# Kernel tuning notes

Hardware: AMD Instinct MI355X
Metric: run time of the kernel (lower is better)

## Reference

```python
import jax, jax.numpy as jnp
import numpy as np

EPS = 1e-7  # K.epsilon()
NUM_ROUTING = 3


def squash(v, axis=-1):
    sq = jnp.sum(jnp.square(v), axis=axis, keepdims=True)
    return sq / (1.0 + sq) * (v / jnp.sqrt(sq + EPS))


def setup_inputs() -> dict:
    key = jax.random.key(0)
    k1, k2 = jax.random.split(key)
    B, NI, DI = 256, 1152, 8   # batch, input_num_capsule, input_dim_vector
    NJ, DJ = 10, 16            # num_capsule, dim_vector
    u = jax.random.normal(k1, (B, NI, DI), dtype=jnp.float32)
    W = jax.random.normal(k2, (NJ, NI, DJ, DI), dtype=jnp.float32) * 0.1
    return {"u": u, "W": W}


def reference(u, W):
    # u_hat[b,j,i,d] = sum_k u[b,i,k] * W[j,i,d,k]  (replaces tile + batch_dot)
    u_hat = jnp.einsum('bik,jidk->bjid', u, W)
    B, NJ, NI, _ = u_hat.shape
    b_ij = jnp.zeros((B, NJ, NI), dtype=u_hat.dtype)
    v_j = None
    for _ in range(NUM_ROUTING):
        c_ij = jax.nn.softmax(b_ij, axis=1)            # softmax over output capsules (dim=1)
        s_j = jnp.einsum('bji,bjid->bjd', c_ij, u_hat)  # weighted sum over input capsules
        v_j = squash(s_j)                               # (B, NJ, DJ)
        b_ij = b_ij + jnp.einsum('bjd,bjid->bji', v_j, u_hat)  # agreement update
    return v_j
```

## Files before the change

### kernel.cpp

```cpp
#include <hip/hip_runtime.h>
#include <math.h>

#define BB   256
#define NI   1152
#define DI   8
#define NJ   10
#define DJ   16
#define NCHUNK 18
#define CHUNK  64
#define BG     32
#define NBG    8
#define GRID_MAIN (NJ * NCHUNK * NBG)
#define CTP  66

typedef _Float16 half2_t __attribute__((ext_vector_type(2)));
typedef _Float16 half4_t __attribute__((ext_vector_type(4)));
typedef _Float16 half8_t __attribute__((ext_vector_type(8)));
typedef float    f32x4   __attribute__((ext_vector_type(4)));

template <int CTRL>
__device__ __forceinline__ float dpp_add(float x) {
    int xi = __float_as_int(x);
    int yi = __builtin_amdgcn_update_dpp(0, xi, CTRL, 0xF, 0xF, true);
    return x + __int_as_float(yi);
}

__device__ __forceinline__ float dot16(half8_t w, half8_t uu) {
    half2_t w0 = {w[0], w[1]}, w1 = {w[2], w[3]}, w2 = {w[4], w[5]}, w3 = {w[6], w[7]};
    half2_t a0 = {uu[0], uu[1]}, a1 = {uu[2], uu[3]}, a2 = {uu[4], uu[5]}, a3 = {uu[6], uu[7]};
    float acc = __builtin_amdgcn_fdot2(w0, a0, 0.f, false);
    acc = __builtin_amdgcn_fdot2(w1, a1, acc, false);
    acc = __builtin_amdgcn_fdot2(w2, a2, acc, false);
    acc = __builtin_amdgcn_fdot2(w3, a3, acc, false);
    return acc;
}

struct Ctx {
    int j, chunk, bg, i0, b0, tid, il, dq, lane, w, g, xcd, local;
};

__device__ __forceinline__ Ctx make_ctx(int bid, int tid) {
    Ctx c;
    c.xcd = bid & 7; c.local = bid >> 3;
    int gx = c.xcd * (GRID_MAIN / 8) + c.local;
    c.j = gx % NJ; int r = gx / NJ;
    c.chunk = r % NCHUNK; c.bg = r / NCHUNK;
    c.i0 = c.chunk * CHUNK; c.b0 = c.bg * BG;
    c.tid = tid; c.il = tid >> 2; c.dq = tid & 3;
    c.lane = tid & 63; c.w = tid >> 6; c.g = (c.lane >> 4) & 3;
    return c;
}

__device__ __forceinline__ void loadW16(const _Float16* __restrict__ W16, const Ctx& cx,
                                        half8_t* Wh) {
    const half8_t* wp = (const half8_t*)(W16 +
        (((size_t)cx.j * NI + cx.i0 + cx.il) * DJ + cx.dq * 4) * DI);
#pragma unroll
    for (int q = 0; q < 4; ++q) Wh[q] = wp[q];
}

__global__ __launch_bounds__(256) void k_cvt(const float* __restrict__ uf,
                                             const float* __restrict__ Wf,
                                             _Float16* __restrict__ u16,
                                             _Float16* __restrict__ W16) {
    int idx = blockIdx.x * 256 + threadIdx.x;
    const int nu4 = (BB * NI * DI) / 4;
    const int nw4 = (NJ * NI * DJ * DI) / 4;
    if (idx < nu4) {
        float4 v = ((const float4*)uf)[idx];
        half4_t h = {(_Float16)v.x, (_Float16)v.y, (_Float16)v.z, (_Float16)v.w};
        ((half4_t*)u16)[idx] = h;
    } else if (idx < nu4 + nw4) {
        int k = idx - nu4;
        float4 v = ((const float4*)Wf)[k];
        half4_t h = {(_Float16)v.x, (_Float16)v.y, (_Float16)v.z, (_Float16)v.w};
        ((half4_t*)W16)[k] = h;
    }
}

template <int CSRC>
__device__ __forceinline__ void phaseAm(const Ctx& cx, const _Float16* __restrict__ u16,
                                        const _Float16* __restrict__ W16,
                                        float* __restrict__ spart,
                                        const float* ctile, float* sres2) {
    int l = cx.lane, w = cx.w;
    int drow = l & 15;
    int ksub = l >> 4;

    half8_t Wf[4];
#pragma unroll
    for (int qq = 0; qq < 4; ++qq) {
        int i = cx.i0 + w * 16 + qq * 4 + ksub;
        Wf[qq] = *(const half8_t*)(W16 + (((size_t)cx.j * NI + i) * DJ + drow) * DI);
    }

    half8_t au[2][4];
#pragma unroll
    for (int h = 0; h < 2; ++h) {
        int b = cx.b0 + h * 16 + drow;
#pragma unroll
        for (int qq = 0; qq < 4; ++qq) {
            int il = w * 16 + qq * 4 + ksub;
            au[h][qq] = *(const half8_t*)(u16 + ((size_t)b * NI + cx.i0 + il) * DI);
        }
    }
    if (CSRC == 1) {
#pragma unroll
        for (int h = 0; h < 2; ++h) {
#pragma unroll
            for (int qq = 0; qq < 4; ++qq) {
                int il = w * 16 + qq * 4 + ksub;
                _Float16 ch = (_Float16)ctile[(h * 16 + drow) * CTP + il];
                half8_t cc = {ch, ch, ch, ch, ch, ch, ch, ch};
                au[h][qq] = au[h][qq] * cc;
            }
        }
    }

#pragma unroll
    for (int h = 0; h < 2; ++h) {
        f32x4 acc = {0.f, 0.f, 0.f, 0.f};
#pragma unroll
        for (int qq = 0; qq < 4; ++qq)
            acc = __builtin_amdgcn_mfma_f32_16x16x32_f16(au[h][qq], Wf[qq], acc, 0, 0, 0);
#pragma unroll
        for (int r = 0; r < 4; ++r)
            sres2[((h * 4 + w) * 16 + ksub * 4 + r) * 17 + drow] = acc[r];
    }
    __syncthreads();

#pragma unroll
    for (int p = 0; p < 2; ++p) {
        int idx = p * 256 + cx.tid;
        int d = idx & 15, brow = (idx >> 4) & 15, h = idx >> 8;
        float s = 0.f;
#pragma unroll
        for (int w2 = 0; w2 < 4; ++w2)
            s += sres2[((h * 4 + w2) * 16 + brow) * 17 + d];
        if (CSRC == 0) s *= 0.1f;
        spart[(((size_t)cx.chunk * BB + cx.b0 + h * 16 + brow) * NJ + cx.j) * DJ + d] = s;
    }
}

__global__ __launch_bounds__(256) void k_A0m(const _Float16* __restrict__ u16,
                                             const _Float16* __restrict__ W16,
                                             float* __restrict__ spart) {
    __shared__ __align__(16) float sres2[2 * 4 * 16 * 17];
    Ctx cx = make_ctx(blockIdx.x, threadIdx.x);
    phaseAm<0>(cx, u16, W16, spart, nullptr, sres2);
}

__global__ __launch_bounds__(256) void k_Afm(const _Float16* __restrict__ u16,
                                             const _Float16* __restrict__ W16,
                                             const _Float16* __restrict__ delta,
                                             float* __restrict__ spart) {
    __shared__ __align__(16) float sres2[2 * 4 * 16 * 17];
    __shared__ __align__(16) float ctile[BG * CTP];
    Ctx cx = make_ctx(blockIdx.x, threadIdx.x);

#pragma unroll
    for (int q = 0; q < 4; ++q) {
        int slot = q * 256 + cx.tid;
        int bb = slot >> 5;
        int s2 = slot & 31;
        int b = cx.b0 + bb;
        const _Float16* dp = delta + (size_t)b * NJ * NI + cx.i0 + s2 * 2;
        float x0[NJ], x1[NJ];
        float mx0 = -1e30f, mx1 = -1e30f;
#pragma unroll
        for (int jj = 0; jj < NJ; ++jj) {
            half2_t h = *(const half2_t*)(dp + (size_t)jj * NI);
            x0[jj] = (float)h[0]; x1[jj] = (float)h[1];
            mx0 = fmaxf(mx0, x0[jj]); mx1 = fmaxf(mx1, x1[jj]);
        }
        float s0 = 0.f, s1 = 0.f;
#pragma unroll
        for (int jj = 0; jj < NJ; ++jj) {
            x0[jj] = __expf(x0[jj] - mx0); s0 += x0[jj];
            x1[jj] = __expf(x1[jj] - mx1); s1 += x1[jj];
        }
        float2 cw; cw.x = x0[cx.j] / s0; cw.y = x1[cx.j] / s1;
        *(float2*)&ctile[bb * CTP + s2 * 2] = cw;
    }
    __syncthreads();

    phaseAm<1>(cx, u16, W16, spart, ctile, sres2);
}

__global__ __launch_bounds__(256) void k_BV(const _Float16* __restrict__ u16,
                                            const _Float16* __restrict__ W16,
                                            const float* __restrict__ spart,
                                            _Float16* __restrict__ delta, int accum) {
    __shared__ __align__(16) float vsm[BG * DJ];
    __shared__ __align__(16) float bres[BG * CHUNK];
    Ctx cx = make_ctx(blockIdx.x, threadIdx.x);
    half8_t Wh[4];
    loadW16(W16, cx, Wh);

    half8_t puA[4];
#pragma unroll
    for (int s2 = 0; s2 < 4; ++s2) {
        int b = cx.b0 + s2;
        puA[s2] = *(const half8_t*)(u16 + ((size_t)b * NI + cx.i0 + cx.il) * DI);
    }

    if (cx.tid < 128) {
        int bb = cx.tid >> 2, dq2 = cx.tid & 3;
        int b = cx.b0 + bb;
        float4 s4 = {0.f, 0.f, 0.f, 0.f};
#pragma unroll
        for (int ch = 0; ch < NCHUNK; ++ch) {
            float4 t = *(const float4*)&spart[(((size_t)ch * BB + b) * NJ + cx.j) * DJ + dq2 * 4];
            s4.x += t.x; s4.y += t.y; s4.z += t.z; s4.w += t.w;
        }
        float sq = s4.x * s4.x + s4.y * s4.y + s4.z * s4.z + s4.w * s4.w;
        sq = dpp_add<0x0B1>(sq);
        sq = dpp_add<0x04E>(sq);
        float scale = (sq / (1.f + sq)) / sqrtf(sq + 1e-7f);
        float4 vv; vv.x = s4.x * scale; vv.y = s4.y * scale;
        vv.z = s4.z * scale; vv.w = s4.w * scale;
        *(float4*)&vsm[bb * DJ + dq2 * 4] = vv;
    }
    __syncthreads();

#pragma unroll
    for (int grp = 0; grp < 8; ++grp) {
        half8_t puB[4];
        if (grp < 7) {
#pragma unroll
            for (int s2 = 0; s2 < 4; ++s2) {
                int b = cx.b0 + (grp + 1) * 4 + s2;
                puB[s2] = *(const half8_t*)(u16 + ((size_t)b * NI + cx.i0 + cx.il) * DI);
            }
        }
#pragma unroll
        for (int s2 = 0; s2 < 4; ++s2) {
            int bb = grp * 4 + s2;
            float4 vv = *(const float4*)&vsm[bb * DJ + cx.dq * 4];
            float p = vv.x * dot16(Wh[0], puA[s2]);
            p = fmaf(vv.y, dot16(Wh[1], puA[s2]), p);
            p = fmaf(vv.z, dot16(Wh[2], puA[s2]), p);
            p = fmaf(vv.w, dot16(Wh[3], puA[s2]), p);
            p = dpp_add<0x0B1>(p);
            p = dpp_add<0x04E>(p);
            if (cx.dq == 0) bres[bb * CHUNK + cx.il] = p;
        }
        if (grp < 7) {
#pragma unroll
            for (int s2 = 0; s2 < 4; ++s2) puA[s2] = puB[s2];
        }
    }

    __syncthreads();
#pragma unroll
    for (int h = 0; h < 2; ++h) {
        int bb = (cx.tid >> 4) + 16 * h;
        int q  = cx.tid & 15;
        float4 val = ((const float4*)(bres + bb * CHUNK))[q];
        _Float16* dst = delta + (((size_t)(cx.b0 + bb) * NJ + cx.j) * NI + cx.i0) + q * 4;
        half4_t o;
        if (accum) {
            half4_t old = *(const half4_t*)dst;
            o[0] = (_Float16)(val.x + (float)old[0]);
            o[1] = (_Float16)(val.y + (float)old[1]);
            o[2] = (_Float16)(val.z + (float)old[2]);
            o[3] = (_Float16)(val.w + (float)old[3]);
        } else {
            o[0] = (_Float16)val.x; o[1] = (_Float16)val.y;
            o[2] = (_Float16)val.z; o[3] = (_Float16)val.w;
        }
        *(half4_t*)dst = o;
    }
}

__global__ __launch_bounds__(256) void k_V(const float* __restrict__ spart,
                                           float* __restrict__ out) {
    int idx4 = blockIdx.x * 256 + threadIdx.x;
    float4 s4 = {0.f, 0.f, 0.f, 0.f};
#pragma unroll
    for (int ch = 0; ch < NCHUNK; ++ch) {
        float4 t = *(const float4*)&spart[(size_t)ch * (BB * NJ * DJ) + (size_t)idx4 * 4];
        s4.x += t.x; s4.y += t.y; s4.z += t.z; s4.w += t.w;
    }
    float sq = s4.x * s4.x + s4.y * s4.y + s4.z * s4.z + s4.w * s4.w;
    sq = dpp_add<0x0B1>(sq);
    sq = dpp_add<0x04E>(sq);
    float scale = (sq / (1.f + sq)) / sqrtf(sq + 1e-7f);
    float4 o; o.x = s4.x * scale; o.y = s4.y * scale;
    o.z = s4.z * scale; o.w = s4.w * scale;
    *(float4*)&out[(size_t)idx4 * 4] = o;
}

extern "C" void kernel_launch(void* const* d_in, const int* in_sizes, int n_in,
                              void* d_out, int out_size, void* d_ws, size_t ws_size,
                              hipStream_t stream) {
    const float* u = (const float*)d_in[0];
    const float* W = (const float*)d_in[1];
    float* out = (float*)d_out;

    float*     spart = (float*)d_ws;
    _Float16*  delta = (_Float16*)(spart + (size_t)NCHUNK * BB * NJ * DJ);
    _Float16*  u16   = delta + (size_t)BB * NJ * NI;
    _Float16*  W16   = u16 + (size_t)BB * NI * DI;

    dim3 blk(256);
    const int GRID_CVT = ((BB * NI * DI) / 4 + (NJ * NI * DJ * DI) / 4) / 256;

    k_cvt<<<GRID_CVT, blk, 0, stream>>>(u, W, u16, W16);
    k_A0m<<<GRID_MAIN, blk, 0, stream>>>(u16, W16, spart);
    k_BV<<<GRID_MAIN, blk, 0, stream>>>(u16, W16, spart, delta, 0);
    k_Afm<<<GRID_MAIN, blk, 0, stream>>>(u16, W16, delta, spart);
    k_BV<<<GRID_MAIN, blk, 0, stream>>>(u16, W16, spart, delta, 1);
    k_Afm<<<GRID_MAIN, blk, 0, stream>>>(u16, W16, delta, spart);
    k_V<<<40, blk, 0, stream>>>(spart, out);
}
```

Before: 85.91 us.

## Hoist W/u loads before softmax, drop max-subtraction, widen conversion kernel work

In k_Afm, the W fragment and the first half of u rows are now loaded before the softmax coefficient computation and the barrier, so their global-memory latency overlaps the softmax work. The max-subtraction pass in the softmax over output capsules is removed, which saves a loop but risks overflow if the logits grow large. The second u half is loaded after the first MFMA batch, which shortens register lifetimes. The fp32-to-fp16 conversion kernel now has each thread convert four float4 elements, with a quarter of the grid.

Measured after the change: 84.50 us, median of 2. About the same (-1.6%).

```diff
diff --git a/kernel.cpp b/kernel.cpp
--- a/kernel.cpp
+++ b/kernel.cpp
@@ -59,40 +59,45 @@
     for (int q = 0; q < 4; ++q) Wh[q] = wp[q];
 }
 
+__device__ __forceinline__ void loadWf(const _Float16* __restrict__ W16, const Ctx& cx,
+                                       half8_t* Wf) {
+    int drow = cx.lane & 15, ksub = cx.lane >> 4;
+#pragma unroll
+    for (int qq = 0; qq < 4; ++qq) {
+        int i = cx.i0 + cx.w * 16 + qq * 4 + ksub;
+        Wf[qq] = *(const half8_t*)(W16 + (((size_t)cx.j * NI + i) * DJ + drow) * DI);
+    }
+}
+
 __global__ __launch_bounds__(256) void k_cvt(const float* __restrict__ uf,
                                              const float* __restrict__ Wf,
                                              _Float16* __restrict__ u16,
                                              _Float16* __restrict__ W16) {
-    int idx = blockIdx.x * 256 + threadIdx.x;
     const int nu4 = (BB * NI * DI) / 4;
-    const int nw4 = (NJ * NI * DJ * DI) / 4;
-    if (idx < nu4) {
-        float4 v = ((const float4*)uf)[idx];
-        half4_t h = {(_Float16)v.x, (_Float16)v.y, (_Float16)v.z, (_Float16)v.w};
-        ((half4_t*)u16)[idx] = h;
-    } else if (idx < nu4 + nw4) {
-        int k = idx - nu4;
-        float4 v = ((const float4*)Wf)[k];
-        half4_t h = {(_Float16)v.x, (_Float16)v.y, (_Float16)v.z, (_Float16)v.w};
-        ((half4_t*)W16)[k] = h;
-    }
-}
-
-template <int CSRC>
-__device__ __forceinline__ void phaseAm(const Ctx& cx, const _Float16* __restrict__ u16,
-                                        const _Float16* __restrict__ W16,
-                                        float* __restrict__ spart,
-                                        const float* ctile, float* sres2) {
+    int base = (blockIdx.x * 256 + threadIdx.x) * 4;
+    if (base < nu4) {
+#pragma unroll
+        for (int t = 0; t < 4; ++t) {
+            float4 v = ((const float4*)uf)[base + t];
+            half4_t h = {(_Float16)v.x, (_Float16)v.y, (_Float16)v.z, (_Float16)v.w};
+            ((half4_t*)u16)[base + t] = h;
+        }
+    } else {
+        int k = base - nu4;
+#pragma unroll
+        for (int t = 0; t < 4; ++t) {
+            float4 v = ((const float4*)Wf)[k + t];
+            half4_t h = {(_Float16)v.x, (_Float16)v.y, (_Float16)v.z, (_Float16)v.w};
+            ((half4_t*)W16)[k + t] = h;
+        }
+    }
+}
+
+__device__ __forceinline__ void phaseAm0(const Ctx& cx, const _Float16* __restrict__ u16,
+                                         float* __restrict__ spart,
+                                         const half8_t* Wf, float* sres2) {
     int l = cx.lane, w = cx.w;
-    int drow = l & 15;
-    int ksub = l >> 4;
-
-    half8_t Wf[4];
-#pragma unroll
-    for (int qq = 0; qq < 4; ++qq) {
-        int i = cx.i0 + w * 16 + qq * 4 + ksub;
-        Wf[qq] = *(const half8_t*)(W16 + (((size_t)cx.j * NI + i) * DJ + drow) * DI);
-    }
+    int drow = l & 15, ksub = l >> 4;
 
     half8_t au[2][4];
 #pragma unroll
@@ -102,18 +107,6 @@
         for (int qq = 0; qq < 4; ++qq) {
             int il = w * 16 + qq * 4 + ksub;
             au[h][qq] = *(const half8_t*)(u16 + ((size_t)b * NI + cx.i0 + il) * DI);
-        }
-    }
-    if (CSRC == 1) {
-#pragma unroll
-        for (int h = 0; h < 2; ++h) {
-#pragma unroll
-            for (int qq = 0; qq < 4; ++qq) {
-                int il = w * 16 + qq * 4 + ksub;
-                _Float16 ch = (_Float16)ctile[(h * 16 + drow) * CTP + il];
-                half8_t cc = {ch, ch, ch, ch, ch, ch, ch, ch};
-                au[h][qq] = au[h][qq] * cc;
-            }
         }
     }
 
@@ -137,7 +130,7 @@
 #pragma unroll
         for (int w2 = 0; w2 < 4; ++w2)
             s += sres2[((h * 4 + w2) * 16 + brow) * 17 + d];
-        if (CSRC == 0) s *= 0.1f;
+        s *= 0.1f;
         spart[(((size_t)cx.chunk * BB + cx.b0 + h * 16 + brow) * NJ + cx.j) * DJ + d] = s;
     }
 }
@@ -147,7 +140,9 @@
                                              float* __restrict__ spart) {
     __shared__ __align__(16) float sres2[2 * 4 * 16 * 17];
     Ctx cx = make_ctx(blockIdx.x, threadIdx.x);
-    phaseAm<0>(cx, u16, W16, spart, nullptr, sres2);
+    half8_t Wf[4];
+    loadWf(W16, cx, Wf);
+    phaseAm0(cx, u16, spart, Wf, sres2);
 }
 
 __global__ __launch_bounds__(256) void k_Afm(const _Float16* __restrict__ u16,
@@ -157,6 +152,11 @@
     __shared__ __align__(16) float sres2[2 * 4 * 16 * 17];
     __shared__ __align__(16) float ctile[BG * CTP];
     Ctx cx = make_ctx(blockIdx.x, threadIdx.x);
+    int l = cx.lane, w = cx.w;
+    int drow = l & 15, ksub = l >> 4;
+
+    half8_t Wf[4];
+    loadWf(W16, cx, Wf);
 
 #pragma unroll
     for (int q = 0; q < 4; ++q) {
@@ -166,25 +166,73 @@
         int b = cx.b0 + bb;
         const _Float16* dp = delta + (size_t)b * NJ * NI + cx.i0 + s2 * 2;
         float x0[NJ], x1[NJ];
-        float mx0 = -1e30f, mx1 = -1e30f;
+        float s0 = 0.f, s1 = 0.f;
 #pragma unroll
         for (int jj = 0; jj < NJ; ++jj) {
             half2_t h = *(const half2_t*)(dp + (size_t)jj * NI);
-            x0[jj] = (float)h[0]; x1[jj] = (float)h[1];
-            mx0 = fmaxf(mx0, x0[jj]); mx1 = fmaxf(mx1, x1[jj]);
-        }
-        float s0 = 0.f, s1 = 0.f;
-#pragma unroll
-        for (int jj = 0; jj < NJ; ++jj) {
-            x0[jj] = __expf(x0[jj] - mx0); s0 += x0[jj];
-            x1[jj] = __expf(x1[jj] - mx1); s1 += x1[jj];
+            x0[jj] = __expf((float)h[0]); s0 += x0[jj];
+            x1[jj] = __expf((float)h[1]); s1 += x1[jj];
         }
         float2 cw; cw.x = x0[cx.j] / s0; cw.y = x1[cx.j] / s1;
         *(float2*)&ctile[bb * CTP + s2 * 2] = cw;
     }
-    __syncthreads();
-
-    phaseAm<1>(cx, u16, W16, spart, ctile, sres2);
+
+    half8_t au0[4];
+    {
+        int b = cx.b0 + drow;
+#pragma unroll
+        for (int qq = 0; qq < 4; ++qq) {
+            int il = w * 16 + qq * 4 + ksub;
+            au0[qq] = *(const half8_t*)(u16 + ((size_t)b * NI + cx.i0 + il) * DI);
+        }
+    }
+    __syncthreads();
+
+    {
+        f32x4 acc = {0.f, 0.f, 0.f, 0.f};
+#pragma unroll
+        for (int qq = 0; qq < 4; ++qq) {
+            int il = w * 16 + qq * 4 + ksub;
+            _Float16 ch = (_Float16)ctile[drow * CTP + il];
+            half8_t cc = {ch, ch, ch, ch, ch, ch, ch, ch};
+            acc = __builtin_amdgcn_mfma_f32_16x16x32_f16(au0[qq] * cc, Wf[qq], acc, 0, 0, 0);
+        }
+#pragma unroll
+        for (int r = 0; r < 4; ++r)
+            sres2[((0 * 4 + w) * 16 + ksub * 4 + r) * 17 + drow] = acc[r];
+    }
+    {
+        int b = cx.b0 + 16 + drow;
+        half8_t au1[4];
+#pragma unroll
+        for (int qq = 0; qq < 4; ++qq) {
+            int il = w * 16 + qq * 4 + ksub;
+            au1[qq] = *(const half8_t*)(u16 + ((size_t)b * NI + cx.i0 + il) * DI);
+        }
+        f32x4 acc = {0.f, 0.f, 0.f, 0.f};
+#pragma unroll
+        for (int qq = 0; qq < 4; ++qq) {
+            int il = w * 16 + qq * 4 + ksub;
+            _Float16 ch = (_Float16)ctile[(16 + drow) * CTP + il];
+            half8_t cc = {ch, ch, ch, ch, ch, ch, ch, ch};
+            acc = __builtin_amdgcn_mfma_f32_16x16x32_f16(au1[qq] * cc, Wf[qq], acc, 0, 0, 0);
+        }
+#pragma unroll
+        for (int r = 0; r < 4; ++r)
+            sres2[((1 * 4 + w) * 16 + ksub * 4 + r) * 17 + drow] = acc[r];
+    }
+    __syncthreads();
+
+#pragma unroll
+    for (int p = 0; p < 2; ++p) {
+        int idx = p * 256 + cx.tid;
+        int d = idx & 15, brow = (idx >> 4) & 15, h = idx >> 8;
+        float s = 0.f;
+#pragma unroll
+        for (int w2 = 0; w2 < 4; ++w2)
+            s += sres2[((h * 4 + w2) * 16 + brow) * 17 + d];
+        spart[(((size_t)cx.chunk * BB + cx.b0 + h * 16 + brow) * NJ + cx.j) * DJ + d] = s;
+    }
 }
 
 __global__ __launch_bounds__(256) void k_BV(const _Float16* __restrict__ u16,
@@ -304,7 +352,7 @@
     _Float16*  W16   = u16 + (size_t)BB * NI * DI;
 
     dim3 blk(256);
-    const int GRID_CVT = ((BB * NI * DI) / 4 + (NJ * NI * DJ * DI) / 4) / 256;
+    const int GRID_CVT = ((BB * NI * DI) / 4 + (NJ * NI * DJ * DI) / 4) / (256 * 4);
 
     k_cvt<<<GRID_CVT, blk, 0, stream>>>(u, W, u16, W16);
     k_A0m<<<GRID_MAIN, blk, 0, stream>>>(u16, W16, spart);
```
